# Kernel optimization log

Measured on AMD Instinct MI355X. Metric: run time of the kernel, lower is better.

## Reference

```python
import jax, jax.numpy as jnp
import numpy as np

N_STEPS = 2
S_MAX = 3.0
BUDGET = 32.0

def _unit(x):
    n = jnp.linalg.norm(x, axis=-1, keepdims=True)
    return x / jnp.maximum(n, 1e-12)

def setup_inputs() -> dict:
    key = jax.random.key(0)
    ks = jax.random.split(key, 12)
    BS, B, M, D, N = 8, 4, 2048, 128, 1024
    seed = jax.random.normal(ks[0], (BS, N, D), jnp.float32)
    w_cand = jax.random.normal(ks[1], (BS, N, D), jnp.float32)
    novelty = jax.random.uniform(ks[2], (BS, N), jnp.float32)
    g_em = jax.random.uniform(ks[3], (BS,), jnp.float32)
    em_K = _unit(jax.random.normal(ks[4], (BS, B, M, D), jnp.float32))
    em_V = jax.random.normal(ks[5], (BS, B, M, D), jnp.float32)
    em_S = jax.random.uniform(ks[6], (BS, B, M), jnp.float32)
    em_age = jax.random.uniform(ks[7], (BS, B, M), jnp.float32)
    w1 = jax.random.normal(ks[8], (B, D), jnp.float32) * 0.02
    w2 = jax.random.normal(ks[9], (B, D), jnp.float32) * 0.02
    gate_bias = jnp.zeros((B, D), jnp.float32)
    raw_tau = jnp.zeros((B,), jnp.float32)
    raw_tau_w = jnp.zeros((B,), jnp.float32)
    return dict(seed=seed, w_cand=w_cand, novelty=novelty, g_em=g_em,
                em_K=em_K, em_V=em_V, em_S=em_S, em_age=em_age,
                w1=w1, w2=w2, gate_bias=gate_bias,
                raw_tau=raw_tau, raw_tau_w=raw_tau_w, b=0)

def reference(seed, w_cand, novelty, g_em, em_K, em_V, em_S, em_age,
              w1, w2, gate_bias, raw_tau, raw_tau_w, b):
    Kb = em_K[:, b]          # [BS, M, D]
    Vb = em_V[:, b]          # [BS, M, D]
    Sb = em_S[:, b]          # [BS, M]
    ageb = em_age[:, b]      # [BS, M]
    active = (Sb > 0)[:, None, :]  # [BS, 1, M]

    # ---- trail_read (eval mode: no sigma noise) ----
    tau = jax.nn.softplus(raw_tau[b]) + 0.1
    y = seed
    for _ in range(N_STEPS):
        scores = jnp.einsum('bnd,bmd->bnm', y, Kb) / tau
        scores = jnp.where(active, scores, -jnp.inf)
        attn = jnp.nan_to_num(jax.nn.softmax(scores, axis=-1), nan=0.0)
        delta = jnp.einsum('bnm,bmd->bnd', attn, Vb)
        gate = jax.nn.sigmoid(w1[b] * y + w2[b] * delta + gate_bias[b])
        y = y + gate * delta
    y_em = y - seed

    # ---- commit: soft routing -> aggregate -> neuromodulated EMA ----
    tau_w = jax.nn.softplus(raw_tau_w[b]) + 0.1
    M_slots = Kb.shape[1]
    w_norm = _unit(w_cand)
    route_scores = jnp.einsum('bnd,bmd->bnm', w_norm, Kb) / tau_w
    route_scores = jnp.where(active, route_scores, -jnp.inf)
    route = jnp.nan_to_num(jax.nn.softmax(route_scores, axis=-1), nan=1.0 / M_slots)
    weighted_route = novelty[..., None] * route           # [BS, N, M]
    route_agg = weighted_route.mean(axis=1)               # [BS, M]
    denom = jnp.maximum(weighted_route.sum(axis=1), 1e-8)[..., None]  # [BS, M, 1]
    update_K = jnp.einsum('bnm,bnd->bmd', weighted_route, w_norm) / denom
    update_V = jnp.einsum('bnm,bnd->bmd', weighted_route, w_cand) / denom
    alpha = jnp.minimum(g_em[:, None] * route_agg, 1.0)   # [BS, M]
    a = alpha[..., None]
    new_K = (1 - a) * Kb + a * _unit(update_K)
    new_V = (1 - a) * Vb + a * update_V
    new_S = jnp.clip(Sb + alpha, 0.0, S_MAX)
    new_age = ageb * (1 - alpha)
    # budget_enforce: rescale strengths so each row sums to at most BUDGET
    scale = jnp.minimum(1.0, BUDGET / jnp.maximum(new_S.sum(-1, keepdims=True), 1e-8))
    new_S = new_S * scale
    return (y_em, new_K, new_V, new_S, new_age)
```

## Files before the change

kernel.cpp:

```cpp
#include <hip/hip_runtime.h>
#include <hip/hip_bf16.h>
#include <math.h>

#define BS_ 8
#define B_  4
#define M_  2048
#define D_  128
#define N_  1024
#define NEG (-1e30f)

typedef unsigned short us_t;
typedef __attribute__((ext_vector_type(8))) short bf8v;
typedef __attribute__((ext_vector_type(4))) float f4v;

__device__ __forceinline__ float softplus_(float x) {
    return (x > 20.0f) ? x : log1pf(expf(x));
}
__device__ __forceinline__ float dot4_acc(float4 a, float4 b, float acc) {
    acc = fmaf(a.x, b.x, acc);
    acc = fmaf(a.y, b.y, acc);
    acc = fmaf(a.z, b.z, acc);
    acc = fmaf(a.w, b.w, acc);
    return acc;
}
__device__ __forceinline__ us_t f2bf(float x) {
    __hip_bfloat16 h = __float2bfloat16(x);
    return __builtin_bit_cast(us_t, h);
}
__device__ __forceinline__ float bf2f(us_t u) {
    unsigned v = ((unsigned)u) << 16;
    return __builtin_bit_cast(float, v);
}
__device__ __forceinline__ int swz(int us_idx, int row) { return us_idx ^ ((row & 7) << 3); }

__global__ __launch_bounds__(256, 2) void conv_k(
    const float* __restrict__ w_cand, const float* __restrict__ emK,
    const float* __restrict__ emV, const int* __restrict__ bp,
    us_t* __restrict__ Kbf, us_t* __restrict__ Wcg,
    us_t* __restrict__ WcTg, us_t* __restrict__ Vtg, float* __restrict__ invnW)
{
    __shared__ float wt[64][132];
    __shared__ float invn[64];
    const int tid = threadIdx.x;
    const int bs  = blockIdx.y;
    const int bx  = blockIdx.x;
    const int b   = bp[0];

    if (bx < 32) {
        const float* src = emK + ((size_t)(bs * B_ + b)) * M_ * D_ + (size_t)bx * 64 * D_;
        us_t* dst = Kbf + (size_t)bs * M_ * D_ + (size_t)bx * 64 * D_;
        for (int i = tid; i < 64 * 128 / 4; i += 256) {
            float4 v = ((const float4*)src)[i];
            ushort4 o;
            o.x = f2bf(v.x); o.y = f2bf(v.y); o.z = f2bf(v.z); o.w = f2bf(v.w);
            ((ushort4*)dst)[i] = o;
        }
        return;
    }
    if (bx >= 48) {
        const int m0 = (bx - 48) * 64;
        const float* Vb = emV + ((size_t)(bs * B_ + b)) * M_ * D_ + (size_t)m0 * D_;
        for (int c = tid; c < 64 * 32; c += 256) {
            int row = c >> 5, col = (c & 31) << 2;
            *(float4*)&wt[row][col] = *(const float4*)&Vb[row * D_ + col];
        }
        __syncthreads();
        us_t* VtB = Vtg + (size_t)bs * D_ * M_;
        for (int c = tid; c < 1024; c += 256) {
            int d = c >> 3, mc = c & 7;
            uint4 o;
            o.x = (unsigned)f2bf(wt[mc * 8 + 0][d]) | ((unsigned)f2bf(wt[mc * 8 + 1][d]) << 16);
            o.y = (unsigned)f2bf(wt[mc * 8 + 2][d]) | ((unsigned)f2bf(wt[mc * 8 + 3][d]) << 16);
            o.z = (unsigned)f2bf(wt[mc * 8 + 4][d]) | ((unsigned)f2bf(wt[mc * 8 + 5][d]) << 16);
            o.w = (unsigned)f2bf(wt[mc * 8 + 6][d]) | ((unsigned)f2bf(wt[mc * 8 + 7][d]) << 16);
            *(uint4*)&VtB[(size_t)d * M_ + m0 + mc * 8] = o;
        }
        return;
    }
    const int n0 = (bx - 32) * 64;
    const float* Wb = w_cand + (size_t)bs * N_ * D_ + (size_t)n0 * D_;
    for (int c = tid; c < 64 * 32; c += 256) {
        int row = c >> 5, col = (c & 31) << 2;
        *(float4*)&wt[row][col] = *(const float4*)&Wb[row * D_ + col];
    }
    __syncthreads();
    {
        int r = tid >> 2, j = tid & 3;
        float ss = 0.0f;
        #pragma unroll
        for (int q = 0; q < 8; ++q) {
            float4 v = *(float4*)&wt[r][q * 16 + j * 4];
            ss = dot4_acc(v, v, ss);
        }
        ss += __shfl_xor(ss, 1, 4);
        ss += __shfl_xor(ss, 2, 4);
        if (j == 0) invn[r] = 1.0f / fmaxf(sqrtf(ss), 1e-12f);
    }
    __syncthreads();
    us_t* WcB = Wcg + (size_t)bs * N_ * D_ + (size_t)n0 * D_;
    for (int e = tid; e < 8192; e += 256) {
        int row = e >> 7, col = e & 127;
        WcB[row * D_ + col] = f2bf(wt[row][col]);
    }
    us_t* WcTB = WcTg + (size_t)bs * D_ * N_;
    for (int e = tid; e < 8192; e += 256) {
        int d = e >> 6, n = e & 63;
        WcTB[d * N_ + n0 + n] = f2bf(wt[n][d]);
    }
    if (tid < 64) invnW[(size_t)bs * N_ + n0 + tid] = invn[tid];
}

__global__ __launch_bounds__(256, 2) void attn_part_k(
    const float* __restrict__ ySrc, const us_t* __restrict__ Kbf,
    const us_t* __restrict__ Vtg, const float* __restrict__ emS,
    const float* __restrict__ raw_tau, const int* __restrict__ bp,
    us_t* __restrict__ pDelta, float2* __restrict__ pML)
{
    __shared__ us_t KtL[2][8192];
    __shared__ us_t VtL[2][8192];
    __shared__ us_t Pl[4][1024];
    __shared__ float sbt[2][64];

    const int tid = threadIdx.x;
    const int raw = blockIdx.x;
    const int logical = (raw & 7) * 64 + (raw >> 3);
    const int bs = logical >> 6;
    const int rem = logical & 63;
    const int nt = rem >> 2;
    const int q  = rem & 3;
    const int b = bp[0];
    const float rtau = 1.0f / (softplus_(raw_tau[b]) + 0.1f);

    const us_t* KbB = Kbf + (size_t)bs * M_ * D_ + (size_t)(q * 512) * D_;
    const us_t* VtB = Vtg + (size_t)bs * D_ * M_;
    const float* SbB = emS + ((size_t)(bs * B_ + b)) * M_ + q * 512;

    const int wave = tid >> 6, lane = tid & 63;
    const int r = lane & 15, kg = lane >> 4;

    bf8v yb[4];
    {
        const float* yrow = ySrc + ((size_t)bs * N_ + nt * 64 + wave * 16 + r) * D_;
        #pragma unroll
        for (int kk = 0; kk < 4; ++kk) {
            float4 a = *(const float4*)&yrow[kk * 32 + kg * 8];
            float4 c = *(const float4*)&yrow[kk * 32 + kg * 8 + 4];
            bf8v t;
            t[0] = (short)f2bf(a.x); t[1] = (short)f2bf(a.y);
            t[2] = (short)f2bf(a.z); t[3] = (short)f2bf(a.w);
            t[4] = (short)f2bf(c.x); t[5] = (short)f2bf(c.y);
            t[6] = (short)f2bf(c.z); t[7] = (short)f2bf(c.w);
            yb[kk] = t;
        }
    }

    uint4 kr[4], vr[4];
    float sreg = 0.0f;

#define AP_LOAD(t) do {                                                           \
        for (int i = 0; i < 4; ++i) {                                             \
            int c = tid + i * 256;                                                \
            kr[i] = *(const uint4*)&KbB[(size_t)((t) * 64 + (c >> 4)) * D_ + ((c & 15) << 3)]; \
            vr[i] = *(const uint4*)&VtB[(size_t)(c >> 3) * M_ + q * 512 + (t) * 64 + ((c & 7) << 3)]; \
        }                                                                         \
        if (tid < 64) sreg = SbB[(t) * 64 + tid];                                 \
    } while (0)

#define AP_WRITE(bf) do {                                                         \
        for (int i = 0; i < 4; ++i) {                                             \
            int c = tid + i * 256;                                                \
            int ki = (c >> 4) * 128 + ((c & 15) << 3);                            \
            *(uint4*)&KtL[bf][swz(ki, c >> 4)] = kr[i];                           \
            int vi = (c >> 3) * 64 + ((c & 7) << 3);                              \
            *(uint4*)&VtL[bf][swz(vi, c >> 3)] = vr[i];                           \
        }                                                                         \
        if (tid < 64) sbt[bf][tid] = sreg;                                        \
    } while (0)

    f4v cD[8];
    #pragma unroll
    for (int df = 0; df < 8; ++df) cD[df] = (f4v){0.f, 0.f, 0.f, 0.f};
    float mrun = NEG, lsum = 0.0f;

    AP_LOAD(0);
    AP_WRITE(0);
    __syncthreads();

    for (int t = 0; t < 8; ++t) {
        const int cur = t & 1;
        if (t < 7) AP_LOAD(t + 1);

        float sv[4][4];
        #pragma unroll
        for (int mf = 0; mf < 4; ++mf) {
            f4v c4 = {0.f, 0.f, 0.f, 0.f};
            #pragma unroll
            for (int kk = 0; kk < 4; ++kk) {
                int row_ = mf * 16 + r;
                bf8v a = *(bf8v*)&KtL[cur][swz(row_ * 128 + kk * 32 + kg * 8, row_)];
                c4 = __builtin_amdgcn_mfma_f32_16x16x32_bf16(a, yb[kk], c4, 0, 0, 0);
            }
            #pragma unroll
            for (int reg = 0; reg < 4; ++reg) {
                int ml = mf * 16 + kg * 4 + reg;
                sv[mf][reg] = (sbt[cur][ml] > 0.0f) ? c4[reg] * rtau : NEG;
            }
        }
        float tmax = NEG;
        #pragma unroll
        for (int mf = 0; mf < 4; ++mf)
            #pragma unroll
            for (int reg = 0; reg < 4; ++reg) tmax = fmaxf(tmax, sv[mf][reg]);
        tmax = fmaxf(tmax, __shfl_xor(tmax, 16, 64));
        tmax = fmaxf(tmax, __shfl_xor(tmax, 32, 64));
        float mnew = fmaxf(mrun, tmax);
        float f = (mnew > -1e29f) ? __expf(mrun - mnew) : 1.0f;
        mrun = mnew;

        float psum = 0.0f;
        #pragma unroll
        for (int mf = 0; mf < 4; ++mf)
            #pragma unroll
            for (int reg = 0; reg < 4; ++reg) {
                float p = (sv[mf][reg] > -1e29f) ? __expf(sv[mf][reg] - mnew) : 0.0f;
                psum += p;
                int ml = mf * 16 + kg * 4 + reg;
                Pl[wave][swz(r * 64 + ml, r)] = f2bf(p);
            }
        lsum = lsum * f + psum;

        float fr[4];
        #pragma unroll
        for (int reg = 0; reg < 4; ++reg) fr[reg] = __shfl(f, kg * 4 + reg, 64);
        #pragma unroll
        for (int df = 0; df < 8; ++df)
            #pragma unroll
            for (int reg = 0; reg < 4; ++reg) cD[df][reg] *= fr[reg];

        #pragma unroll
        for (int kk = 0; kk < 2; ++kk) {
            bf8v pa = *(bf8v*)&Pl[wave][swz(r * 64 + kk * 32 + kg * 8, r)];
            #pragma unroll
            for (int df = 0; df < 8; ++df) {
                int row_ = df * 16 + r;
                bf8v bv = *(bf8v*)&VtL[cur][swz(row_ * 64 + kk * 32 + kg * 8, row_)];
                cD[df] = __builtin_amdgcn_mfma_f32_16x16x32_bf16(pa, bv, cD[df], 0, 0, 0);
            }
        }

        if (t < 7) AP_WRITE(cur ^ 1);
        __syncthreads();
    }
#undef AP_LOAD
#undef AP_WRITE

    lsum += __shfl_xor(lsum, 16, 64);
    lsum += __shfl_xor(lsum, 32, 64);
    float invl = (lsum > 0.0f) ? 1.0f / lsum : 0.0f;

    us_t* pd = pDelta + ((size_t)((bs * 16 + nt) * 4 + q)) * (64 * 128);
    #pragma unroll
    for (int reg = 0; reg < 4; ++reg) {
        float il = __shfl(invl, kg * 4 + reg, 64);
        int nrow = wave * 16 + kg * 4 + reg;
        #pragma unroll
        for (int df = 0; df < 8; ++df)
            pd[nrow * 128 + df * 16 + r] = f2bf(cD[df][reg] * il);
    }
    if (kg == 0) {
        int nrow = wave * 16 + r;
        pML[((size_t)((bs * 16 + nt) * 4 + q)) * 64 + nrow] = make_float2(mrun, lsum);
    }
}

__global__ __launch_bounds__(256, 2) void attn_merge_k(
    const float* __restrict__ ySrc, const float* __restrict__ seed,
    const us_t* __restrict__ pDelta, const float2* __restrict__ pML,
    const float* __restrict__ w1, const float* __restrict__ w2,
    const float* __restrict__ gb, const int* __restrict__ bp,
    float* __restrict__ yOut, int mode)
{
    __shared__ float w1L[128], w2L[128], gbL[128];
    const int tid = threadIdx.x, raw = blockIdx.x;
    const int logical = (raw & 7) * 16 + (raw >> 3);
    const int bs = logical >> 4, nt = logical & 15;
    const int b = bp[0];
    if (tid < 128) {
        w1L[tid] = w1[b * D_ + tid];
        w2L[tid] = w2[b * D_ + tid];
        gbL[tid] = gb[b * D_ + tid];
    }
    __syncthreads();
    const int rw = tid >> 2, dj = tid & 3;
    const size_t base = ((size_t)(bs * 16 + nt)) * 4;
    float2 ml0 = pML[(base + 0) * 64 + rw];
    float2 ml1 = pML[(base + 1) * 64 + rw];
    float2 ml2 = pML[(base + 2) * 64 + rw];
    float2 ml3 = pML[(base + 3) * 64 + rw];
    float M = fmaxf(fmaxf(ml0.x, ml1.x), fmaxf(ml2.x, ml3.x));
    float w0 = 0.f, wA = 0.f, wB = 0.f, w3 = 0.f, tot = 0.f;
    if (M > -1e29f) {
        w0 = ml0.y * __expf(ml0.x - M);
        wA = ml1.y * __expf(ml1.x - M);
        wB = ml2.y * __expf(ml2.x - M);
        w3 = ml3.y * __expf(ml3.x - M);
        tot = w0 + wA + wB + w3;
    }
    float inv = (tot > 0.0f) ? 1.0f / tot : 0.0f;
    w0 *= inv; wA *= inv; wB *= inv; w3 *= inv;

    const us_t* pd0 = pDelta + (base + 0) * 8192 + rw * 128;
    const us_t* pd1 = pDelta + (base + 1) * 8192 + rw * 128;
    const us_t* pd2 = pDelta + (base + 2) * 8192 + rw * 128;
    const us_t* pd3 = pDelta + (base + 3) * 8192 + rw * 128;
    const float* yrow = ySrc + ((size_t)bs * N_ + nt * 64 + rw) * D_;
    const float* srow = seed + ((size_t)bs * N_ + nt * 64 + rw) * D_;
    float* orow = yOut + ((size_t)bs * N_ + nt * 64 + rw) * D_;

    #pragma unroll
    for (int e = 0; e < 4; ++e) {
        int d0 = dj * 32 + e * 8;
        uint4 u0 = *(const uint4*)&pd0[d0];
        uint4 u1 = *(const uint4*)&pd1[d0];
        uint4 u2 = *(const uint4*)&pd2[d0];
        uint4 u3 = *(const uint4*)&pd3[d0];
        const us_t* a0 = (const us_t*)&u0;
        const us_t* a1 = (const us_t*)&u1;
        const us_t* a2 = (const us_t*)&u2;
        const us_t* a3 = (const us_t*)&u3;
        float4 ya = *(const float4*)&yrow[d0];
        float4 yc = *(const float4*)&yrow[d0 + 4];
        float yv[8] = {ya.x, ya.y, ya.z, ya.w, yc.x, yc.y, yc.z, yc.w};
        float res[8];
        #pragma unroll
        for (int j = 0; j < 8; ++j) {
            float dl = w0 * bf2f(a0[j]) + wA * bf2f(a1[j]) + wB * bf2f(a2[j]) + w3 * bf2f(a3[j]);
            int d = d0 + j;
            float g = 1.0f / (1.0f + __expf(-(w1L[d] * yv[j] + w2L[d] * dl + gbL[d])));
            res[j] = yv[j] + g * dl;
        }
        if (mode == 1) {
            float4 sa = *(const float4*)&srow[d0];
            float4 sc = *(const float4*)&srow[d0 + 4];
            res[0] -= sa.x; res[1] -= sa.y; res[2] -= sa.z; res[3] -= sa.w;
            res[4] -= sc.x; res[5] -= sc.y; res[6] -= sc.z; res[7] -= sc.w;
        }
        float4 o1; o1.x = res[0]; o1.y = res[1]; o1.z = res[2]; o1.w = res[3];
        float4 o2; o2.x = res[4]; o2.y = res[5]; o2.z = res[6]; o2.w = res[7];
        *(float4*)&orow[d0] = o1;
        *(float4*)&orow[d0 + 4] = o2;
    }
}

__global__ __launch_bounds__(256, 2) void stats_k(
    const us_t* __restrict__ Wcg, const us_t* __restrict__ Kbf,
    const float* __restrict__ invnW, const float* __restrict__ emS,
    const float* __restrict__ raw_tau_w, const int* __restrict__ bp,
    float* __restrict__ mxW, float* __restrict__ smW)
{
    __shared__ us_t KtL[2][8192];
    __shared__ float sbt[2][64];

    const int tid = threadIdx.x;
    const int raw = blockIdx.x;
    const int logical = (raw & 7) * 64 + (raw >> 3);
    const int bs = logical >> 6;
    const int rem = logical & 63;
    const int nt = rem >> 2;
    const int q  = rem & 3;
    const int b = bp[0];
    const float rtw = 1.0f / (softplus_(raw_tau_w[b]) + 0.1f);

    const us_t* KbB = Kbf + (size_t)bs * M_ * D_ + (size_t)(q * 512) * D_;
    const float* SbB = emS + ((size_t)(bs * B_ + b)) * M_ + q * 512;

    const int wave = tid >> 6, lane = tid & 63;
    const int r = lane & 15, kg = lane >> 4;
    const int n = nt * 64 + wave * 16 + r;

    bf8v wb[4];
    {
        const us_t* wrow = Wcg + ((size_t)bs * N_ + n) * D_;
        #pragma unroll
        for (int kk = 0; kk < 4; ++kk)
            wb[kk] = *(const bf8v*)&wrow[kk * 32 + kg * 8];
    }
    const float ivn = invnW[(size_t)bs * N_ + n];

    uint4 kr[4];
    float sreg = 0.0f;

#define ST_LOAD(t) do {                                                           \
        for (int i = 0; i < 4; ++i) {                                             \
            int c = tid + i * 256;                                                \
            kr[i] = *(const uint4*)&KbB[(size_t)((t) * 64 + (c >> 4)) * D_ + ((c & 15) << 3)]; \
        }                                                                         \
        if (tid < 64) sreg = SbB[(t) * 64 + tid];                                 \
    } while (0)

#define ST_WRITE(bf) do {                                                         \
        for (int i = 0; i < 4; ++i) {                                             \
            int c = tid + i * 256;                                                \
            int ki = (c >> 4) * 128 + ((c & 15) << 3);                            \
            *(uint4*)&KtL[bf][swz(ki, c >> 4)] = kr[i];                           \
        }                                                                         \
        if (tid < 64) sbt[bf][tid] = sreg;                                        \
    } while (0)

    float mx = NEG, sm = 0.0f;

    ST_LOAD(0);
    ST_WRITE(0);
    __syncthreads();

    for (int t = 0; t < 8; ++t) {
        const int cur = t & 1;
        if (t < 7) ST_LOAD(t + 1);

        #pragma unroll
        for (int mf = 0; mf < 4; ++mf) {
            f4v c4 = {0.f, 0.f, 0.f, 0.f};
            #pragma unroll
            for (int kk = 0; kk < 4; ++kk) {
                int row_ = mf * 16 + r;
                bf8v a = *(bf8v*)&KtL[cur][swz(row_ * 128 + kk * 32 + kg * 8, row_)];
                c4 = __builtin_amdgcn_mfma_f32_16x16x32_bf16(a, wb[kk], c4, 0, 0, 0);
            }
            float v[4]; bool act[4];
            float lm = NEG;
            #pragma unroll
            for (int reg = 0; reg < 4; ++reg) {
                int ml = mf * 16 + kg * 4 + reg;
                v[reg] = c4[reg] * ivn * rtw;
                act[reg] = (sbt[cur][ml] > 0.0f);
                if (act[reg]) lm = fmaxf(lm, v[reg]);
            }
            float mnew = fmaxf(mx, lm);
            if (mnew > -1e29f) {
                float acc = sm * __expf(mx - mnew);
                #pragma unroll
                for (int reg = 0; reg < 4; ++reg)
                    if (act[reg]) acc += __expf(v[reg] - mnew);
                sm = acc; mx = mnew;
            }
        }

        if (t < 7) ST_WRITE(cur ^ 1);
        __syncthreads();
    }
#undef ST_LOAD
#undef ST_WRITE

    #pragma unroll
    for (int off = 16; off <= 32; off <<= 1) {
        float omx = __shfl_xor(mx, off, 64);
        float osm = __shfl_xor(sm, off, 64);
        float nm = fmaxf(mx, omx);
        if (nm > -1e29f) sm = sm * __expf(mx - nm) + osm * __expf(omx - nm);
        else sm = 0.0f;
        mx = nm;
    }
    if (kg == 0) {
        mxW[(size_t)(q * BS_ + bs) * N_ + n] = mx;
        smW[(size_t)(q * BS_ + bs) * N_ + n] = sm;
    }
}

__global__ __launch_bounds__(256) void stats_fin_k(
    const float* __restrict__ mxW, const float* __restrict__ smW,
    const float* __restrict__ novelty,
    float* __restrict__ mxF, float* __restrict__ rivF, float* __restrict__ punF)
{
    int idx = blockIdx.x * 256 + threadIdx.x;
    float m[4], s[4];
    #pragma unroll
    for (int q = 0; q < 4; ++q) {
        m[q] = mxW[q * (BS_ * N_) + idx];
        s[q] = smW[q * (BS_ * N_) + idx];
    }
    float MX = fmaxf(fmaxf(m[0], m[1]), fmaxf(m[2], m[3]));
    float SM = 0.0f;
    if (MX > -1e29f) {
        #pragma unroll
        for (int q = 0; q < 4; ++q)
            if (m[q] > -1e29f) SM += s[q] * __expf(m[q] - MX);
    }
    float nov = novelty[idx];
    if (SM > 0.0f) { mxF[idx] = MX; rivF[idx] = nov / SM; punF[idx] = -1.0f; }
    else           { mxF[idx] = 0.0f; rivF[idx] = 0.0f; punF[idx] = nov * (1.0f / (float)M_); }
}

__global__ __launch_bounds__(256) void update2_k(
    const us_t* __restrict__ Kbf, const us_t* __restrict__ Wcg,
    const us_t* __restrict__ WcTg, const float* __restrict__ g_em,
    const float* __restrict__ emK, const float* __restrict__ emV,
    const float* __restrict__ emS, const float* __restrict__ emAge,
    const float* __restrict__ raw_tau_w, const int* __restrict__ bp,
    const float* __restrict__ invnW, const float* __restrict__ mxF,
    const float* __restrict__ rivF, const float* __restrict__ punF,
    float* __restrict__ outK, float* __restrict__ outV,
    float* __restrict__ outS, float* __restrict__ outA)
{
    __shared__ us_t KaL[8192];
    __shared__ us_t WcL[2][8192];
    __shared__ us_t WcTL[2][8192];
    __shared__ us_t Pl[4096];
    __shared__ us_t P2l[4096];
    __shared__ float4 cns[2][64];
    __shared__ float sbL[64], csL[64], alphaL[64];

    const int tid = threadIdx.x;
    const int raw = blockIdx.x;
    const int logical = (raw & 7) * 32 + (raw >> 3);
    const int bs = logical >> 5;
    const int m0 = (logical & 31) * 64;
    const int b = bp[0];
    const float rtw = 1.0f / (softplus_(raw_tau_w[b]) + 0.1f);
    const float ge = g_em[bs];

    const us_t* KaG = Kbf + (size_t)bs * M_ * D_ + (size_t)m0 * D_;
    const us_t* WcB = Wcg + (size_t)bs * N_ * D_;
    const us_t* WcTB = WcTg + (size_t)bs * D_ * N_;

    for (int c = tid; c < 64 * 16; c += 256) {
        int row = c >> 4, off = (c & 15) << 3;
        uint4 v = *(const uint4*)&KaG[row * 128 + off];
        *(uint4*)&KaL[swz(row * 128 + off, row)] = v;
    }
    if (tid < 64) sbL[tid] = emS[((size_t)(bs * B_ + b)) * M_ + m0 + tid];
    __syncthreads();

    const int wave = tid >> 6, lane = tid & 63;
    const int r = lane & 15, kg = lane >> 4;
    const int mf = wave;

    bf8v a_s[4];
    #pragma unroll
    for (int kk = 0; kk < 4; ++kk) {
        int row = mf * 16 + r;
        a_s[kk] = *(bf8v*)&KaL[swz(row * 128 + kk * 32 + kg * 8, row)];
    }
    bool act4[4];
    #pragma unroll
    for (int reg = 0; reg < 4; ++reg) act4[reg] = (sbL[mf * 16 + kg * 4 + reg] > 0.0f);

    f4v cK[8], cV[8];
    #pragma unroll
    for (int df = 0; df < 8; ++df) { cK[df] = (f4v){0,0,0,0}; cV[df] = (f4v){0,0,0,0}; }
    float csp[4] = {0.f, 0.f, 0.f, 0.f};

    uint4 wr[4], wtr[4];
    float4 creg = {0.f, 0.f, 0.f, 0.f};

#define UP_LOAD(t) do {                                                            \
        for (int i = 0; i < 4; ++i) {                                              \
            int c = tid + i * 256;                                                 \
            wr[i]  = *(const uint4*)&WcB[((size_t)((t) * 64 + (c >> 4))) * D_ + ((c & 15) << 3)]; \
            wtr[i] = *(const uint4*)&WcTB[((size_t)(c >> 3)) * N_ + (t) * 64 + ((c & 7) << 3)];   \
        }                                                                          \
        if (tid < 64) {                                                            \
            int nn = (t) * 64 + tid;                                               \
            creg.x = mxF[(size_t)bs * N_ + nn];                                    \
            creg.y = rivF[(size_t)bs * N_ + nn];                                   \
            creg.z = punF[(size_t)bs * N_ + nn];                                   \
            creg.w = invnW[(size_t)bs * N_ + nn];                                  \
        }                                                                          \
    } while (0)

#define UP_WRITE(bf) do {                                                          \
        for (int i = 0; i < 4; ++i) {                                              \
            int c = tid + i * 256;                                                 \
            int ki = (c >> 4) * 128 + ((c & 15) << 3);                             \
            *(uint4*)&WcL[bf][swz(ki, c >> 4)] = wr[i];                            \
            int vi = (c >> 3) * 64 + ((c & 7) << 3);                               \
            *(uint4*)&WcTL[bf][swz(vi, c >> 3)] = wtr[i];                          \
        }                                                                          \
        if (tid < 64) cns[bf][tid] = creg;                                         \
    } while (0)

    UP_LOAD(0);
    UP_WRITE(0);
    __syncthreads();

    for (int nt = 0; nt < 16; ++nt) {
        const int cur = nt & 1;
        if (nt < 15) UP_LOAD(nt + 1);

        #pragma unroll
        for (int nf = 0; nf < 4; ++nf) {
            f4v c = {0.f, 0.f, 0.f, 0.f};
            #pragma unroll
            for (int kk = 0; kk < 4; ++kk) {
                int row = nf * 16 + r;
                bf8v bb = *(bf8v*)&WcL[cur][swz(row * 128 + kk * 32 + kg * 8, row)];
                c = __builtin_amdgcn_mfma_f32_16x16x32_bf16(a_s[kk], bb, c, 0, 0, 0);
            }
            int nl = nf * 16 + r;
            float4 cn = cns[cur][nl];
            #pragma unroll
            for (int reg = 0; reg < 4; ++reg) {
                float p;
                if (cn.z >= 0.0f) p = cn.z;
                else p = act4[reg] ? cn.y * __expf(c[reg] * cn.w * rtw - cn.x) : 0.0f;
                csp[reg] += p;
                int mrow = mf * 16 + kg * 4 + reg;
                Pl[swz(mrow * 64 + nl, mrow)] = f2bf(p);
                P2l[swz(mrow * 64 + nl, mrow)] = f2bf(p * cn.w);
            }
        }
        #pragma unroll
        for (int kk2 = 0; kk2 < 2; ++kk2) {
            int prow = mf * 16 + r;
            bf8v pa  = *(bf8v*)&Pl[swz(prow * 64 + kk2 * 32 + kg * 8, prow)];
            bf8v pa2 = *(bf8v*)&P2l[swz(prow * 64 + kk2 * 32 + kg * 8, prow)];
            #pragma unroll
            for (int df = 0; df < 8; ++df) {
                int row = df * 16 + r;
                bf8v bw = *(bf8v*)&WcTL[cur][swz(row * 64 + kk2 * 32 + kg * 8, row)];
                cV[df] = __builtin_amdgcn_mfma_f32_16x16x32_bf16(pa, bw, cV[df], 0, 0, 0);
                cK[df] = __builtin_amdgcn_mfma_f32_16x16x32_bf16(pa2, bw, cK[df], 0, 0, 0);
            }
        }

        if (nt < 15) UP_WRITE(cur ^ 1);
        __syncthreads();
    }
#undef UP_LOAD
#undef UP_WRITE

    #pragma unroll
    for (int reg = 0; reg < 4; ++reg) {
        float v = csp[reg];
        v += __shfl_xor(v, 1, 16);
        v += __shfl_xor(v, 2, 16);
        v += __shfl_xor(v, 4, 16);
        v += __shfl_xor(v, 8, 16);
        csp[reg] = v;
    }
    if (r == 0) {
        #pragma unroll
        for (int reg = 0; reg < 4; ++reg) csL[mf * 16 + kg * 4 + reg] = csp[reg];
    }
    __syncthreads();
    if (tid < 64) alphaL[tid] = fminf(ge * csL[tid] * (1.0f / (float)N_), 1.0f);
    __syncthreads();

    float rden[4], nrm[4];
    #pragma unroll
    for (int reg = 0; reg < 4; ++reg) {
        int ml = mf * 16 + kg * 4 + reg;
        rden[reg] = 1.0f / fmaxf(csL[ml], 1e-8f);
        float s = 0.0f;
        #pragma unroll
        for (int df = 0; df < 8; ++df) {
            float u = cK[df][reg] * rden[reg];
            s += u * u;
        }
        s += __shfl_xor(s, 1, 16);
        s += __shfl_xor(s, 2, 16);
        s += __shfl_xor(s, 4, 16);
        s += __shfl_xor(s, 8, 16);
        nrm[reg] = 1.0f / fmaxf(sqrtf(s), 1e-12f);
    }

    const float* KbG = emK + ((size_t)(bs * B_ + b)) * M_ * D_ + (size_t)m0 * D_;
    const float* VbG = emV + ((size_t)(bs * B_ + b)) * M_ * D_ + (size_t)m0 * D_;
    float* oK = outK + (size_t)bs * M_ * D_ + (size_t)m0 * D_;
    float* oV = outV + (size_t)bs * M_ * D_ + (size_t)m0 * D_;
    #pragma unroll
    for (int reg = 0; reg < 4; ++reg) {
        int ml = mf * 16 + kg * 4 + reg;
        float a = alphaL[ml];
        #pragma unroll
        for (int df = 0; df < 8; ++df) {
            int d = df * 16 + r;
            float uK = cK[df][reg] * rden[reg] * nrm[reg];
            float uV = cV[df][reg] * rden[reg];
            oK[ml * D_ + d] = (1.0f - a) * KbG[ml * D_ + d] + a * uK;
            oV[ml * D_ + d] = (1.0f - a) * VbG[ml * D_ + d] + a * uV;
        }
    }
    if (tid < 64) {
        float a = alphaL[tid];
        float sp = fminf(fmaxf(sbL[tid] + a, 0.0f), 3.0f);
        outS[(size_t)bs * M_ + m0 + tid] = sp;
        outA[(size_t)bs * M_ + m0 + tid] =
            emAge[((size_t)(bs * B_ + b)) * M_ + m0 + tid] * (1.0f - a);
    }
}

__global__ __launch_bounds__(256) void scale_s_k(float* __restrict__ outS)
{
    __shared__ float wsum[4];
    const int bs = blockIdx.x, tid = threadIdx.x;
    float* p = outS + (size_t)bs * M_;
    float s = 0.0f;
    for (int i = tid; i < M_; i += 256) s += p[i];
    #pragma unroll
    for (int o = 32; o >= 1; o >>= 1) s += __shfl_xor(s, o, 64);
    if ((tid & 63) == 0) wsum[tid >> 6] = s;
    __syncthreads();
    float tot = wsum[0] + wsum[1] + wsum[2] + wsum[3];
    float scale = fminf(1.0f, 32.0f / fmaxf(tot, 1e-8f));
    for (int i = tid; i < M_; i += 256) p[i] *= scale;
}

extern "C" void kernel_launch(void* const* d_in, const int* in_sizes, int n_in,
                              void* d_out, int out_size, void* d_ws, size_t ws_size,
                              hipStream_t stream) {
    (void)in_sizes; (void)n_in; (void)out_size; (void)ws_size;
    const float* seed    = (const float*)d_in[0];
    const float* w_cand  = (const float*)d_in[1];
    const float* novelty = (const float*)d_in[2];
    const float* g_em    = (const float*)d_in[3];
    const float* emK     = (const float*)d_in[4];
    const float* emV     = (const float*)d_in[5];
    const float* emS     = (const float*)d_in[6];
    const float* emAge   = (const float*)d_in[7];
    const float* w1      = (const float*)d_in[8];
    const float* w2      = (const float*)d_in[9];
    const float* gb      = (const float*)d_in[10];
    const float* rt      = (const float*)d_in[11];
    const float* rtw     = (const float*)d_in[12];
    const int*   bp      = (const int*)d_in[13];

    float* out  = (float*)d_out;
    float* yem  = out;
    float* outK = out + 1048576;
    float* outV = out + 3145728;
    float* outS = out + 5242880;
    float* outA = out + 5259264;

    us_t* Kbf = (us_t*)d_ws;
    us_t* Wcg = Kbf + (size_t)BS_ * M_ * D_;
    us_t* WcT = Wcg + (size_t)BS_ * N_ * D_;
    us_t* Vtg = WcT + (size_t)BS_ * D_ * N_;
    us_t* pDelta = Vtg + (size_t)BS_ * D_ * M_;
    float* fb   = (float*)(pDelta + (size_t)512 * 64 * 128);
    float* invnW = fb;
    float* mxW   = invnW + BS_ * N_;
    float* smW   = mxW + 4 * BS_ * N_;
    float* mxF   = smW + 4 * BS_ * N_;
    float* rivF  = mxF + BS_ * N_;
    float* punF  = rivF + BS_ * N_;
    float* y1    = punF + BS_ * N_;
    float2* pML  = (float2*)(y1 + (size_t)BS_ * N_ * D_);

    conv_k<<<dim3(80, 8), 256, 0, stream>>>(w_cand, emK, emV, bp, Kbf, Wcg, WcT, Vtg, invnW);

    attn_part_k<<<dim3(512), 256, 0, stream>>>(seed, Kbf, Vtg, emS, rt, bp, pDelta, pML);
    attn_merge_k<<<dim3(128), 256, 0, stream>>>(seed, seed, pDelta, pML, w1, w2, gb, bp, y1, 0);
    attn_part_k<<<dim3(512), 256, 0, stream>>>(y1, Kbf, Vtg, emS, rt, bp, pDelta, pML);
    attn_merge_k<<<dim3(128), 256, 0, stream>>>(y1, seed, pDelta, pML, w1, w2, gb, bp, yem, 1);

    stats_k<<<dim3(512), 256, 0, stream>>>(Wcg, Kbf, invnW, emS, rtw, bp, mxW, smW);
    stats_fin_k<<<dim3(32), 256, 0, stream>>>(mxW, smW, novelty, mxF, rivF, punF);
    update2_k<<<dim3(256), 256, 0, stream>>>(Kbf, Wcg, WcT, g_em, emK, emV, emS, emAge,
                                             rtw, bp, invnW, mxF, rivF, punF,
                                             outK, outV, outS, outA);
    scale_s_k<<<8, 256, 0, stream>>>(outS);
}
```

Measured before the change: 268.2 us.

## Drop LDS staging for K/V/W tiles and split update kernel over N halves

```diff
diff --git a/kernel.cpp b/kernel.cpp
--- a/kernel.cpp
+++ b/kernel.cpp
@@ -31,6 +31,7 @@
     unsigned v = ((unsigned)u) << 16;
     return __builtin_bit_cast(float, v);
 }
+__device__ __forceinline__ bf8v gfrag(const us_t* p) { return *(const bf8v*)p; }
 __device__ __forceinline__ int swz(int us_idx, int row) { return us_idx ^ ((row & 7) << 3); }
 
 __global__ __launch_bounds__(256, 2) void conv_k(
@@ -116,10 +117,7 @@
     const float* __restrict__ raw_tau, const int* __restrict__ bp,
     us_t* __restrict__ pDelta, float2* __restrict__ pML)
 {
-    __shared__ us_t KtL[2][8192];
-    __shared__ us_t VtL[2][8192];
     __shared__ us_t Pl[4][1024];
-    __shared__ float sbt[2][64];
 
     const int tid = threadIdx.x;
     const int raw = blockIdx.x;
@@ -137,6 +135,7 @@
 
     const int wave = tid >> 6, lane = tid & 63;
     const int r = lane & 15, kg = lane >> 4;
+    us_t* Pw = Pl[wave];
 
     bf8v yb[4];
     {
@@ -154,56 +153,25 @@
         }
     }
 
-    uint4 kr[4], vr[4];
-    float sreg = 0.0f;
-
-#define AP_LOAD(t) do {                                                           \
-        for (int i = 0; i < 4; ++i) {                                             \
-            int c = tid + i * 256;                                                \
-            kr[i] = *(const uint4*)&KbB[(size_t)((t) * 64 + (c >> 4)) * D_ + ((c & 15) << 3)]; \
-            vr[i] = *(const uint4*)&VtB[(size_t)(c >> 3) * M_ + q * 512 + (t) * 64 + ((c & 7) << 3)]; \
-        }                                                                         \
-        if (tid < 64) sreg = SbB[(t) * 64 + tid];                                 \
-    } while (0)
-
-#define AP_WRITE(bf) do {                                                         \
-        for (int i = 0; i < 4; ++i) {                                             \
-            int c = tid + i * 256;                                                \
-            int ki = (c >> 4) * 128 + ((c & 15) << 3);                            \
-            *(uint4*)&KtL[bf][swz(ki, c >> 4)] = kr[i];                           \
-            int vi = (c >> 3) * 64 + ((c & 7) << 3);                              \
-            *(uint4*)&VtL[bf][swz(vi, c >> 3)] = vr[i];                           \
-        }                                                                         \
-        if (tid < 64) sbt[bf][tid] = sreg;                                        \
-    } while (0)
-
     f4v cD[8];
     #pragma unroll
     for (int df = 0; df < 8; ++df) cD[df] = (f4v){0.f, 0.f, 0.f, 0.f};
     float mrun = NEG, lsum = 0.0f;
 
-    AP_LOAD(0);
-    AP_WRITE(0);
-    __syncthreads();
-
     for (int t = 0; t < 8; ++t) {
-        const int cur = t & 1;
-        if (t < 7) AP_LOAD(t + 1);
-
         float sv[4][4];
         #pragma unroll
         for (int mf = 0; mf < 4; ++mf) {
             f4v c4 = {0.f, 0.f, 0.f, 0.f};
             #pragma unroll
             for (int kk = 0; kk < 4; ++kk) {
-                int row_ = mf * 16 + r;
-                bf8v a = *(bf8v*)&KtL[cur][swz(row_ * 128 + kk * 32 + kg * 8, row_)];
+                bf8v a = gfrag(&KbB[(size_t)(t * 64 + mf * 16 + r) * D_ + kk * 32 + kg * 8]);
                 c4 = __builtin_amdgcn_mfma_f32_16x16x32_bf16(a, yb[kk], c4, 0, 0, 0);
             }
             #pragma unroll
             for (int reg = 0; reg < 4; ++reg) {
-                int ml = mf * 16 + kg * 4 + reg;
-                sv[mf][reg] = (sbt[cur][ml] > 0.0f) ? c4[reg] * rtau : NEG;
+                float sb = SbB[t * 64 + mf * 16 + kg * 4 + reg];
+                sv[mf][reg] = (sb > 0.0f) ? c4[reg] * rtau : NEG;
             }
         }
         float tmax = NEG;
@@ -225,7 +193,7 @@
                 float p = (sv[mf][reg] > -1e29f) ? __expf(sv[mf][reg] - mnew) : 0.0f;
                 psum += p;
                 int ml = mf * 16 + kg * 4 + reg;
-                Pl[wave][swz(r * 64 + ml, r)] = f2bf(p);
+                Pw[swz(r * 64 + ml, r)] = f2bf(p);
             }
         lsum = lsum * f + psum;
 
@@ -239,20 +207,14 @@
 
         #pragma unroll
         for (int kk = 0; kk < 2; ++kk) {
-            bf8v pa = *(bf8v*)&Pl[wave][swz(r * 64 + kk * 32 + kg * 8, r)];
+            bf8v pa = *(bf8v*)&Pw[swz(r * 64 + kk * 32 + kg * 8, r)];
             #pragma unroll
             for (int df = 0; df < 8; ++df) {
-                int row_ = df * 16 + r;
-                bf8v bv = *(bf8v*)&VtL[cur][swz(row_ * 64 + kk * 32 + kg * 8, row_)];
+                bf8v bv = gfrag(&VtB[(size_t)(df * 16 + r) * M_ + q * 512 + t * 64 + kk * 32 + kg * 8]);
                 cD[df] = __builtin_amdgcn_mfma_f32_16x16x32_bf16(pa, bv, cD[df], 0, 0, 0);
             }
         }
-
-        if (t < 7) AP_WRITE(cur ^ 1);
-        __syncthreads();
-    }
-#undef AP_LOAD
-#undef AP_WRITE
+    }
 
     lsum += __shfl_xor(lsum, 16, 64);
     lsum += __shfl_xor(lsum, 32, 64);
@@ -358,9 +320,6 @@
     const float* __restrict__ raw_tau_w, const int* __restrict__ bp,
     float* __restrict__ mxW, float* __restrict__ smW)
 {
-    __shared__ us_t KtL[2][8192];
-    __shared__ float sbt[2][64];
-
     const int tid = threadIdx.x;
     const int raw = blockIdx.x;
     const int logical = (raw & 7) * 64 + (raw >> 3);
@@ -383,56 +342,28 @@
         const us_t* wrow = Wcg + ((size_t)bs * N_ + n) * D_;
         #pragma unroll
         for (int kk = 0; kk < 4; ++kk)
-            wb[kk] = *(const bf8v*)&wrow[kk * 32 + kg * 8];
+            wb[kk] = gfrag(&wrow[kk * 32 + kg * 8]);
     }
     const float ivn = invnW[(size_t)bs * N_ + n];
 
-    uint4 kr[4];
-    float sreg = 0.0f;
-
-#define ST_LOAD(t) do {                                                           \
-        for (int i = 0; i < 4; ++i) {                                             \
-            int c = tid + i * 256;                                                \
-            kr[i] = *(const uint4*)&KbB[(size_t)((t) * 64 + (c >> 4)) * D_ + ((c & 15) << 3)]; \
-        }                                                                         \
-        if (tid < 64) sreg = SbB[(t) * 64 + tid];                                 \
-    } while (0)
-
-#define ST_WRITE(bf) do {                                                         \
-        for (int i = 0; i < 4; ++i) {                                             \
-            int c = tid + i * 256;                                                \
-            int ki = (c >> 4) * 128 + ((c & 15) << 3);                            \
-            *(uint4*)&KtL[bf][swz(ki, c >> 4)] = kr[i];                           \
-        }                                                                         \
-        if (tid < 64) sbt[bf][tid] = sreg;                                        \
-    } while (0)
-
     float mx = NEG, sm = 0.0f;
 
-    ST_LOAD(0);
-    ST_WRITE(0);
-    __syncthreads();
-
     for (int t = 0; t < 8; ++t) {
-        const int cur = t & 1;
-        if (t < 7) ST_LOAD(t + 1);
-
         #pragma unroll
         for (int mf = 0; mf < 4; ++mf) {
             f4v c4 = {0.f, 0.f, 0.f, 0.f};
             #pragma unroll
             for (int kk = 0; kk < 4; ++kk) {
-                int row_ = mf * 16 + r;
-                bf8v a = *(bf8v*)&KtL[cur][swz(row_ * 128 + kk * 32 + kg * 8, row_)];
+                bf8v a = gfrag(&KbB[(size_t)(t * 64 + mf * 16 + r) * D_ + kk * 32 + kg * 8]);
                 c4 = __builtin_amdgcn_mfma_f32_16x16x32_bf16(a, wb[kk], c4, 0, 0, 0);
             }
             float v[4]; bool act[4];
             float lm = NEG;
             #pragma unroll
             for (int reg = 0; reg < 4; ++reg) {
-                int ml = mf * 16 + kg * 4 + reg;
+                float sb = SbB[t * 64 + mf * 16 + kg * 4 + reg];
                 v[reg] = c4[reg] * ivn * rtw;
-                act[reg] = (sbt[cur][ml] > 0.0f);
+                act[reg] = (sb > 0.0f);
                 if (act[reg]) lm = fmaxf(lm, v[reg]);
             }
             float mnew = fmaxf(mx, lm);
@@ -444,13 +375,7 @@
                 sm = acc; mx = mnew;
             }
         }
-
-        if (t < 7) ST_WRITE(cur ^ 1);
-        __syncthreads();
-    }
-#undef ST_LOAD
-#undef ST_WRITE
-
+    }
     #pragma unroll
     for (int off = 16; off <= 32; off <<= 1) {
         float omx = __shfl_xor(mx, off, 64);
@@ -468,8 +393,8 @@
 
 __global__ __launch_bounds__(256) void stats_fin_k(
     const float* __restrict__ mxW, const float* __restrict__ smW,
-    const float* __restrict__ novelty,
-    float* __restrict__ mxF, float* __restrict__ rivF, float* __restrict__ punF)
+    const float* __restrict__ novelty, const float* __restrict__ invnW,
+    float4* __restrict__ cnsG)
 {
     int idx = blockIdx.x * 256 + threadIdx.x;
     float m[4], s[4];
@@ -486,147 +411,122 @@
             if (m[q] > -1e29f) SM += s[q] * __expf(m[q] - MX);
     }
     float nov = novelty[idx];
-    if (SM > 0.0f) { mxF[idx] = MX; rivF[idx] = nov / SM; punF[idx] = -1.0f; }
-    else           { mxF[idx] = 0.0f; rivF[idx] = 0.0f; punF[idx] = nov * (1.0f / (float)M_); }
-}
-
-__global__ __launch_bounds__(256) void update2_k(
+    float4 o;
+    if (SM > 0.0f) { o.x = MX; o.y = nov / SM; o.z = -1.0f; }
+    else           { o.x = 0.0f; o.y = 0.0f; o.z = nov * (1.0f / (float)M_); }
+    o.w = invnW[idx];
+    cnsG[idx] = o;
+}
+
+__global__ __launch_bounds__(256) void update3_k(
     const us_t* __restrict__ Kbf, const us_t* __restrict__ Wcg,
     const us_t* __restrict__ WcTg, const float* __restrict__ g_em,
     const float* __restrict__ emK, const float* __restrict__ emV,
     const float* __restrict__ emS, const float* __restrict__ emAge,
     const float* __restrict__ raw_tau_w, const int* __restrict__ bp,
-    const float* __restrict__ invnW, const float* __restrict__ mxF,
-    const float* __restrict__ rivF, const float* __restrict__ punF,
+    const float4* __restrict__ cnsG,
     float* __restrict__ outK, float* __restrict__ outV,
     float* __restrict__ outS, float* __restrict__ outA)
 {
-    __shared__ us_t KaL[8192];
-    __shared__ us_t WcL[2][8192];
-    __shared__ us_t WcTL[2][8192];
-    __shared__ us_t Pl[4096];
-    __shared__ us_t P2l[4096];
-    __shared__ float4 cns[2][64];
-    __shared__ float sbL[64], csL[64], alphaL[64];
+    __shared__ us_t Pl[4][1024];
+    __shared__ us_t P2l[4][1024];
+    __shared__ f4v partK[2][8][64];
+    __shared__ f4v partV[2][8][64];
+    __shared__ float4 partCs[2][64];
 
     const int tid = threadIdx.x;
     const int raw = blockIdx.x;
-    const int logical = (raw & 7) * 32 + (raw >> 3);
-    const int bs = logical >> 5;
-    const int m0 = (logical & 31) * 64;
+    const int logical = (raw & 7) * 64 + (raw >> 3);
+    const int bs = logical >> 6;
+    const int m0 = (logical & 63) * 32;
     const int b = bp[0];
     const float rtw = 1.0f / (softplus_(raw_tau_w[b]) + 0.1f);
     const float ge = g_em[bs];
 
-    const us_t* KaG = Kbf + (size_t)bs * M_ * D_ + (size_t)m0 * D_;
-    const us_t* WcB = Wcg + (size_t)bs * N_ * D_;
+    const int wave = tid >> 6, lane = tid & 63;
+    const int mf = wave & 1, nh = wave >> 1;
+    const int r = lane & 15, kg = lane >> 4;
+    const int mrow0 = m0 + mf * 16;
+
+    const us_t* WcB  = Wcg + (size_t)bs * N_ * D_;
     const us_t* WcTB = WcTg + (size_t)bs * D_ * N_;
-
-    for (int c = tid; c < 64 * 16; c += 256) {
-        int row = c >> 4, off = (c & 15) << 3;
-        uint4 v = *(const uint4*)&KaG[row * 128 + off];
-        *(uint4*)&KaL[swz(row * 128 + off, row)] = v;
-    }
-    if (tid < 64) sbL[tid] = emS[((size_t)(bs * B_ + b)) * M_ + m0 + tid];
-    __syncthreads();
-
-    const int wave = tid >> 6, lane = tid & 63;
-    const int r = lane & 15, kg = lane >> 4;
-    const int mf = wave;
+    const float4* cnsB = cnsG + (size_t)bs * N_;
+    const float* SbRow = emS + ((size_t)(bs * B_ + b)) * M_ + mrow0;
 
     bf8v a_s[4];
-    #pragma unroll
-    for (int kk = 0; kk < 4; ++kk) {
-        int row = mf * 16 + r;
-        a_s[kk] = *(bf8v*)&KaL[swz(row * 128 + kk * 32 + kg * 8, row)];
+    {
+        const us_t* arow = Kbf + ((size_t)bs * M_ + mrow0 + r) * D_;
+        #pragma unroll
+        for (int kk = 0; kk < 4; ++kk)
+            a_s[kk] = gfrag(&arow[kk * 32 + kg * 8]);
     }
     bool act4[4];
     #pragma unroll
-    for (int reg = 0; reg < 4; ++reg) act4[reg] = (sbL[mf * 16 + kg * 4 + reg] > 0.0f);
+    for (int reg = 0; reg < 4; ++reg) act4[reg] = (SbRow[kg * 4 + reg] > 0.0f);
 
     f4v cK[8], cV[8];
     #pragma unroll
     for (int df = 0; df < 8; ++df) { cK[df] = (f4v){0,0,0,0}; cV[df] = (f4v){0,0,0,0}; }
     float csp[4] = {0.f, 0.f, 0.f, 0.f};
 
-    uint4 wr[4], wtr[4];
-    float4 creg = {0.f, 0.f, 0.f, 0.f};
-
-#define UP_LOAD(t) do {                                                            \
-        for (int i = 0; i < 4; ++i) {                                              \
-            int c = tid + i * 256;                                                 \
-            wr[i]  = *(const uint4*)&WcB[((size_t)((t) * 64 + (c >> 4))) * D_ + ((c & 15) << 3)]; \
-            wtr[i] = *(const uint4*)&WcTB[((size_t)(c >> 3)) * N_ + (t) * 64 + ((c & 7) << 3)];   \
-        }                                                                          \
-        if (tid < 64) {                                                            \
-            int nn = (t) * 64 + tid;                                               \
-            creg.x = mxF[(size_t)bs * N_ + nn];                                    \
-            creg.y = rivF[(size_t)bs * N_ + nn];                                   \
-            creg.z = punF[(size_t)bs * N_ + nn];                                   \
-            creg.w = invnW[(size_t)bs * N_ + nn];                                  \
-        }                                                                          \
-    } while (0)
-
-#define UP_WRITE(bf) do {                                                          \
-        for (int i = 0; i < 4; ++i) {                                              \
-            int c = tid + i * 256;                                                 \
-            int ki = (c >> 4) * 128 + ((c & 15) << 3);                             \
-            *(uint4*)&WcL[bf][swz(ki, c >> 4)] = wr[i];                            \
-            int vi = (c >> 3) * 64 + ((c & 7) << 3);                               \
-            *(uint4*)&WcTL[bf][swz(vi, c >> 3)] = wtr[i];                          \
-        }                                                                          \
-        if (tid < 64) cns[bf][tid] = creg;                                         \
-    } while (0)
-
-    UP_LOAD(0);
-    UP_WRITE(0);
-    __syncthreads();
-
-    for (int nt = 0; nt < 16; ++nt) {
-        const int cur = nt & 1;
-        if (nt < 15) UP_LOAD(nt + 1);
-
+    us_t* Pw = Pl[wave];
+    us_t* P2w = P2l[wave];
+
+    for (int it = 0; it < 8; ++it) {
+        const int n0 = (nh * 8 + it) * 64;
         #pragma unroll
         for (int nf = 0; nf < 4; ++nf) {
             f4v c = {0.f, 0.f, 0.f, 0.f};
             #pragma unroll
             for (int kk = 0; kk < 4; ++kk) {
-                int row = nf * 16 + r;
-                bf8v bb = *(bf8v*)&WcL[cur][swz(row * 128 + kk * 32 + kg * 8, row)];
+                bf8v bb = gfrag(&WcB[(size_t)(n0 + nf * 16 + r) * D_ + kk * 32 + kg * 8]);
                 c = __builtin_amdgcn_mfma_f32_16x16x32_bf16(a_s[kk], bb, c, 0, 0, 0);
             }
-            int nl = nf * 16 + r;
-            float4 cn = cns[cur][nl];
+            float4 cn = cnsB[n0 + nf * 16 + r];
             #pragma unroll
             for (int reg = 0; reg < 4; ++reg) {
                 float p;
                 if (cn.z >= 0.0f) p = cn.z;
                 else p = act4[reg] ? cn.y * __expf(c[reg] * cn.w * rtw - cn.x) : 0.0f;
                 csp[reg] += p;
-                int mrow = mf * 16 + kg * 4 + reg;
-                Pl[swz(mrow * 64 + nl, mrow)] = f2bf(p);
-                P2l[swz(mrow * 64 + nl, mrow)] = f2bf(p * cn.w);
+                int mr = kg * 4 + reg;
+                Pw[swz(mr * 64 + nf * 16 + r, mr)] = f2bf(p);
+                P2w[swz(mr * 64 + nf * 16 + r, mr)] = f2bf(p * cn.w);
             }
         }
         #pragma unroll
         for (int kk2 = 0; kk2 < 2; ++kk2) {
-            int prow = mf * 16 + r;
-            bf8v pa  = *(bf8v*)&Pl[swz(prow * 64 + kk2 * 32 + kg * 8, prow)];
-            bf8v pa2 = *(bf8v*)&P2l[swz(prow * 64 + kk2 * 32 + kg * 8, prow)];
+            bf8v pa  = *(bf8v*)&Pw[swz(r * 64 + kk2 * 32 + kg * 8, r)];
+            bf8v pa2 = *(bf8v*)&P2w[swz(r * 64 + kk2 * 32 + kg * 8, r)];
             #pragma unroll
             for (int df = 0; df < 8; ++df) {
-                int row = df * 16 + r;
-                bf8v bw = *(bf8v*)&WcTL[cur][swz(row * 64 + kk2 * 32 + kg * 8, row)];
+                bf8v bw = gfrag(&WcTB[(size_t)(df * 16 + r) * N_ + n0 + kk2 * 32 + kg * 8]);
                 cV[df] = __builtin_amdgcn_mfma_f32_16x16x32_bf16(pa, bw, cV[df], 0, 0, 0);
                 cK[df] = __builtin_amdgcn_mfma_f32_16x16x32_bf16(pa2, bw, cK[df], 0, 0, 0);
             }
         }
-
-        if (nt < 15) UP_WRITE(cur ^ 1);
-        __syncthreads();
-    }
-#undef UP_LOAD
-#undef UP_WRITE
+    }
+
+    if (nh == 1) {
+        #pragma unroll
+        for (int df = 0; df < 8; ++df) {
+            partK[mf][df][lane] = cK[df];
+            partV[mf][df][lane] = cV[df];
+        }
+        partCs[mf][lane] = make_float4(csp[0], csp[1], csp[2], csp[3]);
+    }
+    __syncthreads();
+    if (nh == 1) return;
+
+    #pragma unroll
+    for (int df = 0; df < 8; ++df) {
+        cK[df] += partK[mf][df][lane];
+        cV[df] += partV[mf][df][lane];
+    }
+    {
+        float4 pc = partCs[mf][lane];
+        csp[0] += pc.x; csp[1] += pc.y; csp[2] += pc.z; csp[3] += pc.w;
+    }
 
     #pragma unroll
     for (int reg = 0; reg < 4; ++reg) {
@@ -637,19 +537,13 @@
         v += __shfl_xor(v, 8, 16);
         csp[reg] = v;
     }
-    if (r == 0) {
-        #pragma unroll
-        for (int reg = 0; reg < 4; ++reg) csL[mf * 16 + kg * 4 + reg] = csp[reg];
-    }
-    __syncthreads();
-    if (tid < 64) alphaL[tid] = fminf(ge * csL[tid] * (1.0f / (float)N_), 1.0f);
-    __syncthreads();
-
-    float rden[4], nrm[4];
+
+    float rden[4], nrm[4], alpha4[4];
     #pragma unroll
     for (int reg = 0; reg < 4; ++reg) {
-        int ml = mf * 16 + kg * 4 + reg;
-        rden[reg] = 1.0f / fmaxf(csL[ml], 1e-8f);
+        float csv = csp[reg];
+        alpha4[reg] = fminf(ge * csv * (1.0f / (float)N_), 1.0f);
+        rden[reg] = 1.0f / fmaxf(csv, 1e-8f);
         float s = 0.0f;
         #pragma unroll
         for (int df = 0; df < 8; ++df) {
@@ -663,29 +557,38 @@
         nrm[reg] = 1.0f / fmaxf(sqrtf(s), 1e-12f);
     }
 
-    const float* KbG = emK + ((size_t)(bs * B_ + b)) * M_ * D_ + (size_t)m0 * D_;
-    const float* VbG = emV + ((size_t)(bs * B_ + b)) * M_ * D_ + (size_t)m0 * D_;
-    float* oK = outK + (size_t)bs * M_ * D_ + (size_t)m0 * D_;
-    float* oV = outV + (size_t)bs * M_ * D_ + (size_t)m0 * D_;
+    const float* KbG = emK + ((size_t)(bs * B_ + b)) * M_ + 0;
+    const float* KbR = emK + ((size_t)(bs * B_ + b)) * M_ * D_ + (size_t)mrow0 * D_;
+    const float* VbR = emV + ((size_t)(bs * B_ + b)) * M_ * D_ + (size_t)mrow0 * D_;
+    (void)KbG;
+    float* oK = outK + (size_t)bs * M_ * D_ + (size_t)mrow0 * D_;
+    float* oV = outV + (size_t)bs * M_ * D_ + (size_t)mrow0 * D_;
     #pragma unroll
     for (int reg = 0; reg < 4; ++reg) {
-        int ml = mf * 16 + kg * 4 + reg;
-        float a = alphaL[ml];
+        int ml = kg * 4 + reg;
+        float a = alpha4[reg];
         #pragma unroll
         for (int df = 0; df < 8; ++df) {
             int d = df * 16 + r;
             float uK = cK[df][reg] * rden[reg] * nrm[reg];
             float uV = cV[df][reg] * rden[reg];
-            oK[ml * D_ + d] = (1.0f - a) * KbG[ml * D_ + d] + a * uK;
-            oV[ml * D_ + d] = (1.0f - a) * VbG[ml * D_ + d] + a * uV;
-        }
-    }
-    if (tid < 64) {
-        float a = alphaL[tid];
-        float sp = fminf(fmaxf(sbL[tid] + a, 0.0f), 3.0f);
-        outS[(size_t)bs * M_ + m0 + tid] = sp;
-        outA[(size_t)bs * M_ + m0 + tid] =
-            emAge[((size_t)(bs * B_ + b)) * M_ + m0 + tid] * (1.0f - a);
+            oK[ml * D_ + d] = (1.0f - a) * KbR[ml * D_ + d] + a * uK;
+            oV[ml * D_ + d] = (1.0f - a) * VbR[ml * D_ + d] + a * uV;
+        }
+    }
+    if (kg == 0) {
+        float cs0 = __shfl(csp[0], (r >> 2) * 16, 64);
+        float cs1 = __shfl(csp[1], (r >> 2) * 16, 64);
+        float cs2 = __shfl(csp[2], (r >> 2) * 16, 64);
+        float cs3 = __shfl(csp[3], (r >> 2) * 16, 64);
+        int sel = r & 3;
+        float csv = (sel == 0) ? cs0 : (sel == 1) ? cs1 : (sel == 2) ? cs2 : cs3;
+        float a = fminf(ge * csv * (1.0f / (float)N_), 1.0f);
+        float sb = SbRow[r];
+        float sp = fminf(fmaxf(sb + a, 0.0f), 3.0f);
+        outS[(size_t)bs * M_ + mrow0 + r] = sp;
+        outA[(size_t)bs * M_ + mrow0 + r] =
+            emAge[((size_t)(bs * B_ + b)) * M_ + mrow0 + r] * (1.0f - a);
     }
 }
 
@@ -736,14 +639,12 @@
     us_t* WcT = Wcg + (size_t)BS_ * N_ * D_;
     us_t* Vtg = WcT + (size_t)BS_ * D_ * N_;
     us_t* pDelta = Vtg + (size_t)BS_ * D_ * M_;
-    float* fb   = (float*)(pDelta + (size_t)512 * 64 * 128);
+    float* fb    = (float*)(pDelta + (size_t)512 * 64 * 128);
     float* invnW = fb;
     float* mxW   = invnW + BS_ * N_;
     float* smW   = mxW + 4 * BS_ * N_;
-    float* mxF   = smW + 4 * BS_ * N_;
-    float* rivF  = mxF + BS_ * N_;
-    float* punF  = rivF + BS_ * N_;
-    float* y1    = punF + BS_ * N_;
+    float4* cnsG = (float4*)(smW + 4 * BS_ * N_);
+    float* y1    = (float*)(cnsG + BS_ * N_);
     float2* pML  = (float2*)(y1 + (size_t)BS_ * N_ * D_);
 
     conv_k<<<dim3(80, 8), 256, 0, stream>>>(w_cand, emK, emV, bp, Kbf, Wcg, WcT, Vtg, invnW);
@@ -754,9 +655,8 @@
     attn_merge_k<<<dim3(128), 256, 0, stream>>>(y1, seed, pDelta, pML, w1, w2, gb, bp, yem, 1);
 
     stats_k<<<dim3(512), 256, 0, stream>>>(Wcg, Kbf, invnW, emS, rtw, bp, mxW, smW);
-    stats_fin_k<<<dim3(32), 256, 0, stream>>>(mxW, smW, novelty, mxF, rivF, punF);
-    update2_k<<<dim3(256), 256, 0, stream>>>(Kbf, Wcg, WcT, g_em, emK, emV, emS, emAge,
-                                             rtw, bp, invnW, mxF, rivF, punF,
-                                             outK, outV, outS, outA);
+    stats_fin_k<<<dim3(32), 256, 0, stream>>>(mxW, smW, novelty, invnW, cnsG);
+    update3_k<<<dim3(512), 256, 0, stream>>>(Kbf, Wcg, WcT, g_em, emK, emV, emS, emAge,
+                                             rtw, bp, cnsG, outK, outV, outS, outA);
     scale_s_k<<<8, 256, 0, stream>>>(outS);
 }
```

After: 401.6 us. 1.5x slower.
